# Kernel optimization log

Hardware: AMD Instinct MI355X
Metric: run time of the kernel (lower is better)

The kernel has to match this reference:

```python
import jax, jax.numpy as jnp
import numpy as np

B, T, D = 4, 2048, 1024
H = 16
HD = D // H


def setup_inputs() -> dict:
    key = jax.random.key(0)
    ks = jax.random.split(key, 9)
    s = 1.0 / np.sqrt(D)
    return {
        "x": jax.random.normal(ks[0], (B, T, D), dtype=jnp.float32),
        "Wk": jax.random.normal(ks[1], (D, D), dtype=jnp.float32) * s,
        "bk": jnp.zeros((D,), dtype=jnp.float32),
        "Wq": jax.random.normal(ks[2], (D, D), dtype=jnp.float32) * s,
        "bq": jnp.zeros((D,), dtype=jnp.float32),
        "Wv": jax.random.normal(ks[3], (D, D), dtype=jnp.float32) * s,
        "bv": jnp.zeros((D,), dtype=jnp.float32),
        "Wp": jax.random.normal(ks[4], (D, D), dtype=jnp.float32) * s,
        "bp": jnp.zeros((D,), dtype=jnp.float32),
    }


def reference(x, Wk, bk, Wq, bq, Wv, bv, Wp, bp):
    Bv, Tv, Dv = x.shape
    # project and split heads: [B, H, T, HD]
    def heads(w, b):
        return (x @ w + b).reshape(Bv, Tv, H, HD).transpose(0, 2, 1, 3)
    k = heads(Wk, bk)
    q = heads(Wq, bq)
    v = heads(Wv, bv)
    scale = 1.0 / np.sqrt(HD)
    att = jnp.einsum('bhqd,bhkd->bhqk', q, k) * scale  # [B,H,T,T]
    causal = jnp.tril(jnp.ones((Tv, Tv), dtype=bool))
    att = jnp.where(causal[None, None, :, :], att, -jnp.inf)
    att = jax.nn.softmax(att, axis=-1)
    y = jnp.einsum('bhqk,bhkd->bhqd', att, v)  # [B,H,T,HD]
    y = y.transpose(0, 2, 1, 3).reshape(Bv, Tv, Dv)
    return y @ Wp + bp
```

## Files before the change

### kernel.cpp

```cpp
#include <hip/hip_runtime.h>
#include <stdint.h>

#define Bb 4
#define Tt 2048
#define Dd 1024
#define Hh 16
#define HDd 64
#define Mm 8192

typedef __attribute__((ext_vector_type(8))) short bf16x8;
typedef __attribute__((ext_vector_type(4))) float f32x4;
typedef __attribute__((ext_vector_type(16))) float f32x16;

#define MFMA(a, b, c) __builtin_amdgcn_mfma_f32_16x16x32_bf16(a, b, c, 0, 0, 0)
#define MFMA32(a, b, c) __builtin_amdgcn_mfma_f32_32x32x16_bf16(a, b, c, 0, 0, 0)

#define LOG2E 1.44269504088896340736f
#if __has_builtin(__builtin_amdgcn_exp2f)
#define EXP2(x) __builtin_amdgcn_exp2f(x)
#else
#define EXP2(x) __expf((x) * 0.69314718055994530942f)
#endif

union vfu { uint2 u2[2]; bf16x8 v; };
union apu { uint32_t u[4]; bf16x8 v; };

__device__ __forceinline__ unsigned short f2b(float f) {
  union { float f; uint32_t u; } v; v.f = f;
  return (unsigned short)((v.u + 0x7FFFu + ((v.u >> 16) & 1u)) >> 16);
}

__device__ __forceinline__ uint32_t pk2(float a, float b) {
  union { __bf16 h[2]; uint32_t u; } x;
  x.h[0] = (__bf16)a; x.h[1] = (__bf16)b;
  return x.u;
}

__device__ __forceinline__ void gload_lds16(const void* g, void* l) {
  __builtin_amdgcn_global_load_lds(
      (const __attribute__((address_space(1))) void*)g,
      (__attribute__((address_space(3))) void*)l, 16, 0, 0);
}

__global__ __launch_bounds__(256) void k_convert_x(const float* __restrict__ x,
                                                   unsigned short* __restrict__ xb) {
  int i = (blockIdx.x * 256 + threadIdx.x) * 8;
  float4 a = *(const float4*)(x + i);
  float4 b = *(const float4*)(x + i + 4);
  uint4 o;
  o.x = f2b(a.x) | ((uint32_t)f2b(a.y) << 16);
  o.y = f2b(a.z) | ((uint32_t)f2b(a.w) << 16);
  o.z = f2b(b.x) | ((uint32_t)f2b(b.y) << 16);
  o.w = f2b(b.z) | ((uint32_t)f2b(b.w) << 16);
  *(uint4*)(xb + i) = o;
}

__global__ __launch_bounds__(256) void k_transpose_w(
    const float* __restrict__ Wk, const float* __restrict__ Wq,
    const float* __restrict__ Wv, const float* __restrict__ Wp,
    unsigned short* __restrict__ WkT, unsigned short* __restrict__ WqT,
    unsigned short* __restrict__ WvT, unsigned short* __restrict__ WpT) {
  const float* W; unsigned short* O;
  int wsel = blockIdx.y;
  W = wsel == 0 ? Wk : wsel == 1 ? Wq : wsel == 2 ? Wv : Wp;
  O = wsel == 0 ? WkT : wsel == 1 ? WqT : wsel == 2 ? WvT : WpT;
  __shared__ unsigned short tile[32][36];
  int kb = (blockIdx.x >> 5) << 5;
  int nb = (blockIdx.x & 31) << 5;
  int t = threadIdx.x;
  int r = t >> 3, c4 = (t & 7) << 2;
  float4 v = *(const float4*)(W + (size_t)(kb + r) * Dd + nb + c4);
  tile[r][c4 + 0] = f2b(v.x); tile[r][c4 + 1] = f2b(v.y);
  tile[r][c4 + 2] = f2b(v.z); tile[r][c4 + 3] = f2b(v.w);
  __syncthreads();
  uint2 o;
  o.x = tile[c4 + 0][r] | ((uint32_t)tile[c4 + 1][r] << 16);
  o.y = tile[c4 + 2][r] | ((uint32_t)tile[c4 + 3][r] << 16);
  *(uint2*)(O + (size_t)(nb + r) * Dd + kb + c4) = o;
}

__global__ __launch_bounds__(256) void k_gemm(
    const unsigned short* __restrict__ A,
    const unsigned short* __restrict__ Bt0, const unsigned short* __restrict__ Bt1,
    const unsigned short* __restrict__ Bt2,
    const float* __restrict__ bias0, const float* __restrict__ bias1,
    const float* __restrict__ bias2,
    unsigned short* __restrict__ Qb, unsigned short* __restrict__ Kb,
    unsigned short* __restrict__ VTb, float* __restrict__ Pout, int qkv) {
  __shared__ __align__(16) unsigned short Al[128 * 32];
  __shared__ __align__(16) unsigned short Bl[128 * 32];
  int tid = threadIdx.x;
  int lane = tid & 63, wid = tid >> 6;
  int wr = wid >> 1, wc = wid & 1;
  int lq = lane & 15, lh = lane >> 4;
  int mb = blockIdx.x * 128;
  int by = blockIdx.y;
  int widx, nb;
  const unsigned short* Bt; const float* bias;
  if (qkv) {
    widx = by >> 3; nb = (by & 7) << 7;
    Bt = widx == 0 ? Bt0 : (widx == 1 ? Bt1 : Bt2);
    bias = widx == 0 ? bias0 : (widx == 1 ? bias1 : bias2);
  } else {
    widx = 3; nb = by << 7; Bt = Bt0; bias = bias0;
  }

  int srow = (wid << 5) + (lane >> 2);
  int scol = (lane & 3) << 3;
  const unsigned short* Ag = A + (size_t)(mb + srow) * Dd + scol;
  const unsigned short* Bg = Bt + (size_t)(nb + srow) * Dd + scol;
  unsigned short* Alw = Al + (wid << 10);
  unsigned short* Blw = Bl + (wid << 10);

  f32x4 zero = {0.f, 0.f, 0.f, 0.f};
  f32x4 acc[4][4];
#pragma unroll
  for (int m = 0; m < 4; m++)
#pragma unroll
    for (int n = 0; n < 4; n++) acc[m][n] = zero;

  for (int kb = 0; kb < Dd; kb += 32) {
    __syncthreads();
    gload_lds16(Ag + kb, Alw);
    gload_lds16(Ag + kb + 16 * Dd, Alw + 16 * 32);
    gload_lds16(Bg + kb, Blw);
    gload_lds16(Bg + kb + 16 * Dd, Blw + 16 * 32);
    __syncthreads();
    bf16x8 af[4], bf[4];
#pragma unroll
    for (int m = 0; m < 4; m++)
      af[m] = *(const bf16x8*)(Al + (((wr << 6) + (m << 4) + lq) << 5) + (lh << 3));
#pragma unroll
    for (int n = 0; n < 4; n++)
      bf[n] = *(const bf16x8*)(Bl + (((wc << 6) + (n << 4) + lq) << 5) + (lh << 3));
#pragma unroll
    for (int m = 0; m < 4; m++)
#pragma unroll
      for (int n = 0; n < 4; n++) acc[m][n] = MFMA(af[m], bf[n], acc[m][n]);
  }

  int b_idx = mb >> 11;
#pragma unroll
  for (int n = 0; n < 4; n++) {
    int col = nb + (wc << 6) + (n << 4) + lq;
    float bb = bias[col];
    int hh = col >> 6, hd = col & 63;
#pragma unroll
    for (int m = 0; m < 4; m++) {
      int row0 = mb + (wr << 6) + (m << 4) + (lh << 2);
      int t0 = row0 & 2047;
      if (widx == 3) {
#pragma unroll
        for (int r = 0; r < 4; r++)
          Pout[(size_t)(row0 + r) * Dd + col] = acc[m][n][r] + bb;
      } else if (widx == 2) {
        float v0 = acc[m][n][0] + bb, v1 = acc[m][n][1] + bb;
        float v2 = acc[m][n][2] + bb, v3 = acc[m][n][3] + bb;
        uint2 pv;
        pv.x = f2b(v0) | ((uint32_t)f2b(v1) << 16);
        pv.y = f2b(v2) | ((uint32_t)f2b(v3) << 16);
        int t0s = t0 ^ ((hd & 7) << 3);
        *(uint2*)(VTb + ((size_t)(b_idx * 16 + hh) * 64 + hd) * Tt + t0s) = pv;
      } else {
        unsigned short* O = (widx == 0) ? Qb : Kb;
        float sc = (widx == 0) ? (0.125f * LOG2E) : 1.0f;
#pragma unroll
        for (int r = 0; r < 4; r++) {
          float v = (acc[m][n][r] + bb) * sc;
          int trow = t0 + r;
          int hds = (widx == 0) ? hd : (hd ^ ((trow & 7) << 3));
          O[((size_t)(b_idx * 16 + hh) * Tt + trow) * 64 + hds] = f2b(v);
        }
      }
    }
  }
}

__global__ __launch_bounds__(256, 2) void k_attn(
    const unsigned short* __restrict__ Qb, const unsigned short* __restrict__ Kb,
    const unsigned short* __restrict__ VTb, unsigned short* __restrict__ yb) {
  __shared__ __align__(16) unsigned short KL[2][4096];
  __shared__ __align__(16) unsigned short VL[2][4096];
  int b = blockIdx.x;
  int qt = (b < 256) ? (7 - (b >> 6)) : ((b - 256) >> 6);
  int rr6 = b & 63;
  int bh = ((rr6 & 7) << 3) | (rr6 >> 3);
  int tid = threadIdx.x, lane = tid & 63, w = tid >> 6;
  int l31 = lane & 31, hi = lane >> 5;
  const unsigned short* __restrict__ Qh = Qb + (size_t)bh * Tt * 64;
  const unsigned short* __restrict__ Kh = Kb + (size_t)bh * Tt * 64;
  const unsigned short* __restrict__ Vh = VTb + (size_t)bh * 64 * Tt;
  int qgA = (qt << 8) + (w << 6);
  int qgB = qgA + 32;

  bf16x8 qfA[4], qfB[4];
#pragma unroll
  for (int c = 0; c < 4; c++) {
    qfA[c] = *(const bf16x8*)(Qh + (size_t)(qgA + l31) * 64 + (c << 4) + (hi << 3));
    qfB[c] = *(const bf16x8*)(Qh + (size_t)(qgB + l31) * 64 + (c << 4) + (hi << 3));
  }

  f32x16 accA0, accA1, accB0, accB1;
#pragma unroll
  for (int i = 0; i < 16; i++) { accA0[i] = 0.f; accA1[i] = 0.f; accB0[i] = 0.f; accB1[i] = 0.f; }
  float lsumA = 0.f, lsumB = 0.f;

  int jmaxb = (qt << 2) + 3;
  int srow = lane >> 3, scol = (lane & 7) << 3;
  int rowb = w << 4;
  int swz = l31 & 7;

#define STAGE(kvt_, bi_) do {                                                       \
    int kv_ = (kvt_) << 6;                                                          \
    gload_lds16(Kh + (size_t)(kv_ + rowb + srow) * 64 + scol, &KL[bi_][rowb << 6]); \
    gload_lds16(Kh + (size_t)(kv_ + rowb + 8 + srow) * 64 + scol,                   \
                &KL[bi_][(rowb + 8) << 6]);                                         \
    gload_lds16(Vh + (size_t)(rowb + srow) * Tt + kv_ + scol, &VL[bi_][rowb << 6]); \
    gload_lds16(Vh + (size_t)(rowb + 8 + srow) * Tt + kv_ + scol,                   \
                &VL[bi_][(rowb + 8) << 6]);                                         \
  } while (0)

  STAGE(0, 0);
  __syncthreads();

  int cur = 0;
  for (int jt = 0; jt <= jmaxb; ++jt) {
    if (jt < jmaxb) STAGE(jt + 1, cur ^ 1);
    int kv0 = jt << 6;
    int dA = qgA - kv0;
    if (dA >= 0) {
      const unsigned short* KB = &KL[cur][0];
      const unsigned short* VB = &VL[cur][0];
      bool dg = (dA == 0);
      int relA = dA + l31, relB = relA + 32;
#pragma unroll
      for (int n2 = 0; n2 < 2; n2++) {
        bf16x8 kf[4];
        int krowb = ((n2 << 5) + l31) << 6;
#pragma unroll
        for (int c = 0; c < 4; c++)
          kf[c] = *(const bf16x8*)(KB + krowb + ((((c << 1) + hi) ^ swz) << 3));
        f32x16 sA, sB;
#pragma unroll
        for (int i = 0; i < 16; i++) { sA[i] = 0.f; sB[i] = 0.f; }
        __builtin_amdgcn_s_setprio(1);
#pragma unroll
        for (int c = 0; c < 4; c++) {
          sA = MFMA32(kf[c], qfA[c], sA);
          sB = MFMA32(kf[c], qfB[c], sB);
        }
        __builtin_amdgcn_s_setprio(0);
        float pA[16], pB[16];
        if (dg) {
#pragma unroll
          for (int r = 0; r < 16; r++) {
            int krow = (n2 << 5) + (r & 3) + ((r >> 2) << 3) + (hi << 2);
            pA[r] = EXP2(krow > relA ? -1e30f : sA[r]);
            pB[r] = EXP2(krow > relB ? -1e30f : sB[r]);
          }
        } else {
#pragma unroll
          for (int r = 0; r < 16; r++) { pA[r] = EXP2(sA[r]); pB[r] = EXP2(sB[r]); }
        }
        lsumA += (((pA[0] + pA[1]) + (pA[2] + pA[3])) + ((pA[4] + pA[5]) + (pA[6] + pA[7])))
               + (((pA[8] + pA[9]) + (pA[10] + pA[11])) + ((pA[12] + pA[13]) + (pA[14] + pA[15])));
        lsumB += (((pB[0] + pB[1]) + (pB[2] + pB[3])) + ((pB[4] + pB[5]) + (pB[6] + pB[7])))
               + (((pB[8] + pB[9]) + (pB[10] + pB[11])) + ((pB[12] + pB[13]) + (pB[14] + pB[15])));
        vfu vf[2][2];
#pragma unroll
        for (int n2v = 0; n2v < 2; n2v++) {
          int vrowb = ((n2v << 5) + l31) << 6;
#pragma unroll
          for (int cc = 0; cc < 2; cc++) {
            int blk0 = (n2 << 2) + (cc << 1);
            vf[n2v][cc].u2[0] =
                *(const uint2*)(VB + vrowb + ((blk0 ^ swz) << 3) + (hi << 2));
            vf[n2v][cc].u2[1] =
                *(const uint2*)(VB + vrowb + (((blk0 + 1) ^ swz) << 3) + (hi << 2));
          }
        }
        apu a0, a1, b0, b1;
#pragma unroll
        for (int g = 0; g < 4; g++) {
          a0.u[g] = pk2(pA[2 * g], pA[2 * g + 1]);
          a1.u[g] = pk2(pA[8 + 2 * g], pA[8 + 2 * g + 1]);
          b0.u[g] = pk2(pB[2 * g], pB[2 * g + 1]);
          b1.u[g] = pk2(pB[8 + 2 * g], pB[8 + 2 * g + 1]);
        }
        __builtin_amdgcn_s_setprio(1);
        accA0 = MFMA32(a0.v, vf[0][0].v, accA0);
        accA1 = MFMA32(a0.v, vf[1][0].v, accA1);
        accB0 = MFMA32(b0.v, vf[0][0].v, accB0);
        accB1 = MFMA32(b0.v, vf[1][0].v, accB1);
        accA0 = MFMA32(a1.v, vf[0][1].v, accA0);
        accA1 = MFMA32(a1.v, vf[1][1].v, accA1);
        accB0 = MFMA32(b1.v, vf[0][1].v, accB0);
        accB1 = MFMA32(b1.v, vf[1][1].v, accB1);
        __builtin_amdgcn_s_setprio(0);
      }
    }
    __syncthreads();
    cur ^= 1;
  }
#undef STAGE

  lsumA += __shfl_xor(lsumA, 32);
  lsumB += __shfl_xor(lsumB, 32);
  float invA = 1.0f / lsumA;
  float invB = 1.0f / lsumB;
  int bb = bh >> 4, hh = bh & 15;
#pragma unroll
  for (int r = 0; r < 16; r++) {
    int qr = (r & 3) + ((r >> 2) << 3) + (hi << 2);
    float invqA = __shfl(invA, qr);
    float invqB = __shfl(invB, qr);
    size_t baseA = ((size_t)(bb * Tt + qgA + qr)) * Dd + (hh << 6) + l31;
    size_t baseB = ((size_t)(bb * Tt + qgB + qr)) * Dd + (hh << 6) + l31;
    yb[baseA] = f2b(accA0[r] * invqA);
    yb[baseA + 32] = f2b(accA1[r] * invqA);
    yb[baseB] = f2b(accB0[r] * invqB);
    yb[baseB + 32] = f2b(accB1[r] * invqB);
  }
}

extern "C" void kernel_launch(void* const* d_in, const int* in_sizes, int n_in,
                              void* d_out, int out_size, void* d_ws, size_t ws_size,
                              hipStream_t stream) {
  const float* x = (const float*)d_in[0];
  const float* Wk = (const float*)d_in[1];
  const float* bk = (const float*)d_in[2];
  const float* Wq = (const float*)d_in[3];
  const float* bq = (const float*)d_in[4];
  const float* Wv = (const float*)d_in[5];
  const float* bv = (const float*)d_in[6];
  const float* Wp = (const float*)d_in[7];
  const float* bp = (const float*)d_in[8];
  float* out = (float*)d_out;

  char* ws = (char*)d_ws;
  unsigned short* xb  = (unsigned short*)(ws);
  unsigned short* WkT = (unsigned short*)(ws + (16ull << 20));
  unsigned short* WqT = (unsigned short*)(ws + (18ull << 20));
  unsigned short* WvT = (unsigned short*)(ws + (20ull << 20));
  unsigned short* WpT = (unsigned short*)(ws + (22ull << 20));
  unsigned short* Qb  = (unsigned short*)(ws + (24ull << 20));
  unsigned short* Kb  = (unsigned short*)(ws + (40ull << 20));
  unsigned short* VTb = (unsigned short*)(ws + (56ull << 20));
  unsigned short* yb  = (unsigned short*)(ws + (72ull << 20));

  k_convert_x<<<4096, 256, 0, stream>>>(x, xb);
  k_transpose_w<<<dim3(1024, 4), 256, 0, stream>>>(Wk, Wq, Wv, Wp, WkT, WqT, WvT, WpT);
  k_gemm<<<dim3(64, 24), 256, 0, stream>>>(xb, WqT, WkT, WvT, bq, bk, bv,
                                           Qb, Kb, VTb, nullptr, 1);
  k_attn<<<512, 256, 0, stream>>>(Qb, Kb, VTb, yb);
  k_gemm<<<dim3(64, 8), 256, 0, stream>>>(yb, WpT, nullptr, nullptr, bp, nullptr, nullptr,
                                          nullptr, nullptr, nullptr, out, 0);
}
```

Before: 187.5 us.

## Fuse Q/K/V projections into one GEMM kernel sharing the A tile

Replaces the 24-column-block QKV GEMM launch with a kernel where each block computes Q, K and V for the same 128x128 output tile, loading the x tile into shared memory once and reusing it across three weight tiles. This cuts redundant global/LDS traffic for the activation matrix and uses s_setprio around the MFMA bursts. The cost is triple the accumulator registers (48 f32x4 per thread) and more LDS, which, despite the launch_bounds(256,2) hint, may cause spills or lower occupancy; the grid also shrinks from 1536 to 512 blocks. The output projection GEMM is simplified to a single-purpose kernel.

```diff
diff --git a/kernel.cpp b/kernel.cpp
--- a/kernel.cpp
+++ b/kernel.cpp
@@ -79,14 +79,115 @@
   *(uint2*)(O + (size_t)(nb + r) * Dd + kb + c4) = o;
 }
 
+__global__ __launch_bounds__(256, 2) void k_gemm3(
+    const unsigned short* __restrict__ A,
+    const unsigned short* __restrict__ BtQ, const unsigned short* __restrict__ BtK,
+    const unsigned short* __restrict__ BtV,
+    const float* __restrict__ bq, const float* __restrict__ bk,
+    const float* __restrict__ bv,
+    unsigned short* __restrict__ Qb, unsigned short* __restrict__ Kb,
+    unsigned short* __restrict__ VTb) {
+  __shared__ __align__(16) unsigned short Al[128 * 32];
+  __shared__ __align__(16) unsigned short Bl[3][128 * 32];
+  int tid = threadIdx.x;
+  int lane = tid & 63, wid = tid >> 6;
+  int wr = wid >> 1, wc = wid & 1;
+  int lq = lane & 15, lh = lane >> 4;
+  int mb = blockIdx.x * 128;
+  int nb = blockIdx.y << 7;
+
+  int srow = (wid << 5) + (lane >> 2);
+  int scol = (lane & 3) << 3;
+  const unsigned short* Ag = A + (size_t)(mb + srow) * Dd + scol;
+  const unsigned short* Bg0 = BtQ + (size_t)(nb + srow) * Dd + scol;
+  const unsigned short* Bg1 = BtK + (size_t)(nb + srow) * Dd + scol;
+  const unsigned short* Bg2 = BtV + (size_t)(nb + srow) * Dd + scol;
+  unsigned short* Alw = Al + (wid << 10);
+  unsigned short* Blw0 = &Bl[0][0] + (wid << 10);
+  unsigned short* Blw1 = &Bl[1][0] + (wid << 10);
+  unsigned short* Blw2 = &Bl[2][0] + (wid << 10);
+
+  f32x4 zero = {0.f, 0.f, 0.f, 0.f};
+  f32x4 acc[3][4][4];
+#pragma unroll
+  for (int s = 0; s < 3; s++)
+#pragma unroll
+    for (int m = 0; m < 4; m++)
+#pragma unroll
+      for (int n = 0; n < 4; n++) acc[s][m][n] = zero;
+
+  for (int kb = 0; kb < Dd; kb += 32) {
+    __syncthreads();
+    gload_lds16(Ag + kb, Alw);
+    gload_lds16(Ag + kb + 16 * Dd, Alw + 16 * 32);
+    gload_lds16(Bg0 + kb, Blw0);
+    gload_lds16(Bg0 + kb + 16 * Dd, Blw0 + 16 * 32);
+    gload_lds16(Bg1 + kb, Blw1);
+    gload_lds16(Bg1 + kb + 16 * Dd, Blw1 + 16 * 32);
+    gload_lds16(Bg2 + kb, Blw2);
+    gload_lds16(Bg2 + kb + 16 * Dd, Blw2 + 16 * 32);
+    __syncthreads();
+    bf16x8 af[4];
+#pragma unroll
+    for (int m = 0; m < 4; m++)
+      af[m] = *(const bf16x8*)(Al + (((wr << 6) + (m << 4) + lq) << 5) + (lh << 3));
+#pragma unroll
+    for (int s = 0; s < 3; s++) {
+      bf16x8 bf[4];
+#pragma unroll
+      for (int n = 0; n < 4; n++)
+        bf[n] = *(const bf16x8*)(&Bl[s][0] +
+                                 (((wc << 6) + (n << 4) + lq) << 5) + (lh << 3));
+      __builtin_amdgcn_s_setprio(1);
+#pragma unroll
+      for (int m = 0; m < 4; m++)
+#pragma unroll
+        for (int n = 0; n < 4; n++) acc[s][m][n] = MFMA(af[m], bf[n], acc[s][m][n]);
+      __builtin_amdgcn_s_setprio(0);
+    }
+  }
+
+  int b_idx = mb >> 11;
+#pragma unroll
+  for (int s = 0; s < 3; s++) {
+#pragma unroll
+    for (int n = 0; n < 4; n++) {
+      int col = nb + (wc << 6) + (n << 4) + lq;
+      float bbias = (s == 0) ? bq[col] : (s == 1) ? bk[col] : bv[col];
+      int hh = col >> 6, hd = col & 63;
+#pragma unroll
+      for (int m = 0; m < 4; m++) {
+        int row0 = mb + (wr << 6) + (m << 4) + (lh << 2);
+        int t0 = row0 & 2047;
+        if (s == 2) {
+          float v0 = acc[s][m][n][0] + bbias, v1 = acc[s][m][n][1] + bbias;
+          float v2 = acc[s][m][n][2] + bbias, v3 = acc[s][m][n][3] + bbias;
+          uint2 pv;
+          pv.x = f2b(v0) | ((uint32_t)f2b(v1) << 16);
+          pv.y = f2b(v2) | ((uint32_t)f2b(v3) << 16);
+          int t0s = t0 ^ ((hd & 7) << 3);
+          *(uint2*)(VTb + ((size_t)(b_idx * 16 + hh) * 64 + hd) * Tt + t0s) = pv;
+        } else {
+          unsigned short* O = (s == 0) ? Qb : Kb;
+          float sc = (s == 0) ? (0.125f * LOG2E) : 1.0f;
+#pragma unroll
+          for (int r = 0; r < 4; r++) {
+            float v = (acc[s][m][n][r] + bbias) * sc;
+            int trow = t0 + r;
+            int hds = (s == 0) ? hd : (hd ^ ((trow & 7) << 3));
+            O[((size_t)(b_idx * 16 + hh) * Tt + trow) * 64 + hds] = f2b(v);
+          }
+        }
+      }
+    }
+  }
+}
+
 __global__ __launch_bounds__(256) void k_gemm(
     const unsigned short* __restrict__ A,
-    const unsigned short* __restrict__ Bt0, const unsigned short* __restrict__ Bt1,
-    const unsigned short* __restrict__ Bt2,
-    const float* __restrict__ bias0, const float* __restrict__ bias1,
-    const float* __restrict__ bias2,
-    unsigned short* __restrict__ Qb, unsigned short* __restrict__ Kb,
-    unsigned short* __restrict__ VTb, float* __restrict__ Pout, int qkv) {
+    const unsigned short* __restrict__ Bt0,
+    const float* __restrict__ bias0,
+    float* __restrict__ Pout) {
   __shared__ __align__(16) unsigned short Al[128 * 32];
   __shared__ __align__(16) unsigned short Bl[128 * 32];
   int tid = threadIdx.x;
@@ -94,16 +195,8 @@
   int wr = wid >> 1, wc = wid & 1;
   int lq = lane & 15, lh = lane >> 4;
   int mb = blockIdx.x * 128;
-  int by = blockIdx.y;
-  int widx, nb;
-  const unsigned short* Bt; const float* bias;
-  if (qkv) {
-    widx = by >> 3; nb = (by & 7) << 7;
-    Bt = widx == 0 ? Bt0 : (widx == 1 ? Bt1 : Bt2);
-    bias = widx == 0 ? bias0 : (widx == 1 ? bias1 : bias2);
-  } else {
-    widx = 3; nb = by << 7; Bt = Bt0; bias = bias0;
-  }
+  int nb = blockIdx.y << 7;
+  const unsigned short* Bt = Bt0; const float* bias = bias0;
 
   int srow = (wid << 5) + (lane >> 2);
   int scol = (lane & 3) << 3;
@@ -139,39 +232,16 @@
       for (int n = 0; n < 4; n++) acc[m][n] = MFMA(af[m], bf[n], acc[m][n]);
   }
 
-  int b_idx = mb >> 11;
 #pragma unroll
   for (int n = 0; n < 4; n++) {
     int col = nb + (wc << 6) + (n << 4) + lq;
     float bb = bias[col];
-    int hh = col >> 6, hd = col & 63;
 #pragma unroll
     for (int m = 0; m < 4; m++) {
       int row0 = mb + (wr << 6) + (m << 4) + (lh << 2);
-      int t0 = row0 & 2047;
-      if (widx == 3) {
-#pragma unroll
-        for (int r = 0; r < 4; r++)
-          Pout[(size_t)(row0 + r) * Dd + col] = acc[m][n][r] + bb;
-      } else if (widx == 2) {
-        float v0 = acc[m][n][0] + bb, v1 = acc[m][n][1] + bb;
-        float v2 = acc[m][n][2] + bb, v3 = acc[m][n][3] + bb;
-        uint2 pv;
-        pv.x = f2b(v0) | ((uint32_t)f2b(v1) << 16);
-        pv.y = f2b(v2) | ((uint32_t)f2b(v3) << 16);
-        int t0s = t0 ^ ((hd & 7) << 3);
-        *(uint2*)(VTb + ((size_t)(b_idx * 16 + hh) * 64 + hd) * Tt + t0s) = pv;
-      } else {
-        unsigned short* O = (widx == 0) ? Qb : Kb;
-        float sc = (widx == 0) ? (0.125f * LOG2E) : 1.0f;
-#pragma unroll
-        for (int r = 0; r < 4; r++) {
-          float v = (acc[m][n][r] + bb) * sc;
-          int trow = t0 + r;
-          int hds = (widx == 0) ? hd : (hd ^ ((trow & 7) << 3));
-          O[((size_t)(b_idx * 16 + hh) * Tt + trow) * 64 + hds] = f2b(v);
-        }
-      }
+#pragma unroll
+      for (int r = 0; r < 4; r++)
+        Pout[(size_t)(row0 + r) * Dd + col] = acc[m][n][r] + bb;
     }
   }
 }
@@ -350,9 +420,8 @@
 
   k_convert_x<<<4096, 256, 0, stream>>>(x, xb);
   k_transpose_w<<<dim3(1024, 4), 256, 0, stream>>>(Wk, Wq, Wv, Wp, WkT, WqT, WvT, WpT);
-  k_gemm<<<dim3(64, 24), 256, 0, stream>>>(xb, WqT, WkT, WvT, bq, bk, bv,
-                                           Qb, Kb, VTb, nullptr, 1);
+  k_gemm3<<<dim3(64, 8), 256, 0, stream>>>(xb, WqT, WkT, WvT, bq, bk, bv,
+                                           Qb, Kb, VTb);
   k_attn<<<512, 256, 0, stream>>>(Qb, Kb, VTb, yb);
-  k_gemm<<<dim3(64, 8), 256, 0, stream>>>(yb, WpT, nullptr, nullptr, bp, nullptr, nullptr,
-                                          nullptr, nullptr, nullptr, out, 0);
-}
+  k_gemm<<<dim3(64, 8), 256, 0, stream>>>(yb, WpT, bp, out);
+}
```

Measured after the change: 165.5 us. 1.13x faster.
